# Kernel optimization log

Hardware: AMD Instinct MI355X
Metric: run time of the kernel (lower is better)

Reference implementation:

```python
import jax, jax.numpy as jnp
import numpy as np

HEAD_DEPTH = 64
CLIP = 10.0
SCALE = float(np.sqrt(HEAD_DEPTH))


def setup_inputs() -> dict:
    key = jax.random.key(0)
    kq, kk, kv, km = jax.random.split(key, 4)
    B, H, S, D = 4, 16, 2048, HEAD_DEPTH
    q = jax.random.normal(kq, (B, H, S, D), dtype=jnp.float32)
    k = jax.random.normal(kk, (B, H, S, D), dtype=jnp.float32)
    v = jax.random.normal(kv, (B, H, S, D), dtype=jnp.float32)
    # mask: (batch, n_nodes, 1) bool; True => key position is masked out
    mask = jax.random.randint(km, (B, S, 1), 0, 2).astype(bool)
    return {"q": q, "k": k, "v": v, "mask": mask}


def reference(q, k, v, mask):
    # logits: (B, H, Sq, Sk)
    logits = jnp.einsum('bhqd,bhkd->bhqk', q, k) / SCALE
    logits = CLIP * jnp.tanh(logits)  # tanh-clip of logits
    # mask (B, N, 1) -> broadcast over heads and query positions: (B, 1, 1, N)
    key_mask = mask[:, None, None, :, 0]
    logits = jnp.where(key_mask, -jnp.inf, logits)
    probs = jax.nn.softmax(logits, axis=-1)
    return jnp.einsum('bhqk,bhkd->bhqd', probs, v)
```

## Files before the change

kernel.cpp:

```cpp
#include <hip/hip_runtime.h>

typedef short bf16x8 __attribute__((ext_vector_type(8), may_alias));
typedef float f32x4 __attribute__((ext_vector_type(4)));
typedef unsigned int u32x4a __attribute__((ext_vector_type(4), may_alias));
typedef unsigned int u32x2a __attribute__((ext_vector_type(2), may_alias));
typedef unsigned short ushort;
typedef unsigned int uint;

#define B_N 4
#define H_N 16
#define S_N 2048
#define D_N 64
#define BQ 128
#define WQ 32
#define KT 64
#define NW 4
#define NBLK (B_N*H_N*(S_N/BQ))
#define TILE_BYTES 32768
#define MAXTILE (S_N/KT)
#define IMG_OFF 32768
#define WS_NEED ((size_t)IMG_OFF + (size_t)B_N*H_N*MAXTILE*TILE_BYTES)

#define MFMA16 __builtin_amdgcn_mfma_f32_16x16x32_bf16

__device__ __forceinline__ uint f2bf(float x){
  uint u = __float_as_uint(x);
  u += 0x7fffu + ((u >> 16) & 1u);
  return u >> 16;
}
__device__ __forceinline__ float bf2f(uint h){
  return __uint_as_float(h << 16);
}
__device__ __forceinline__ int ldsw(int off, int row){
  return off ^ ((row & 7) << 4);
}
__device__ __forceinline__ void gload16(const void* g, void* l){
  __builtin_amdgcn_global_load_lds((const uint __attribute__((address_space(1)))*)g,
                                   (uint __attribute__((address_space(3)))*)l, 16, 0, 0);
}

__global__ __launch_bounds__(256)
void compact_k(const int* __restrict__ Mg, int* __restrict__ cnt_ws,
               ushort* __restrict__ idx_ws)
{
  __shared__ int sws[NW];
  const int b = blockIdx.x;
  const int tid = threadIdx.x, lane = tid & 63, w = tid >> 6;
  const int* mb = Mg + (size_t)b * S_N;
  int kept[8]; int cl = 0; int base = tid * 8;
  #pragma unroll
  for (int i = 0; i < 8; ++i){ kept[i] = (mb[base+i] == 0); cl += kept[i]; }
  int inc = cl;
  #pragma unroll
  for (int d = 1; d < 64; d <<= 1){
    int o = __shfl_up(inc, d);
    if (lane >= d) inc += o;
  }
  if (lane == 63) sws[w] = inc;
  __syncthreads();
  int s0 = sws[0], s1 = sws[1], s2 = sws[2], s3 = sws[3];
  int wo = (w > 0 ? s0 : 0) + (w > 1 ? s1 : 0) + (w > 2 ? s2 : 0);
  int pos = wo + inc - cl;
  #pragma unroll
  for (int i = 0; i < 8; ++i){
    if (kept[i]) idx_ws[b*S_N + pos++] = (ushort)(base + i);
  }
  if (tid == 0) cnt_ws[b] = s0 + s1 + s2 + s3;
}

__global__ __launch_bounds__(256)
void stage_k(const float* __restrict__ Kg, const float* __restrict__ Vg,
             const int* __restrict__ cnt_ws, const ushort* __restrict__ idx_ws,
             char* __restrict__ img)
{
  __shared__ float Vl[64*65];
  const int bid = blockIdx.x;
  const int bh = bid >> 5;
  const int tile = bid & 31;
  const int b = bh >> 4;
  const int cnt = cnt_ws[b];
  const int ntile = (cnt + 63) >> 6;
  if (tile >= ntile) return;
  const int tid = threadIdx.x;
  char* G = img + (size_t)bid * TILE_BYTES;

  const int jrow = tid >> 2, c4 = tid & 3;
  int kk = tile*64 + jrow; if (kk >= cnt) kk = cnt - 1;
  const int sidx = idx_ws[b*S_N + kk];
  const size_t kvbase = (size_t)bh * (size_t)(S_N*D_N);
  const int sw = (jrow & 7) << 4;
  {
    const float4* Kp = (const float4*)(Kg + kvbase + (size_t)sidx*D_N) + c4*4;
    float4 k0 = Kp[0], k1 = Kp[1], k2 = Kp[2], k3 = Kp[3];
    float kv[16] = {k0.x,k0.y,k0.z,k0.w,k1.x,k1.y,k1.z,k1.w,
                    k2.x,k2.y,k2.z,k2.w,k3.x,k3.y,k3.z,k3.w};
    uint h[16], l[16];
    #pragma unroll
    for (int e = 0; e < 16; ++e){
      uint hh = f2bf(kv[e]); h[e] = hh; l[e] = f2bf(kv[e] - bf2f(hh));
    }
    char* r0 = G + jrow*128;
    char* r1 = G + 8192 + jrow*128;
    *(u32x4a*)(r0 + ((c4*32)      ^ sw)) = (u32x4a){h[0]|(h[1]<<16),  h[2]|(h[3]<<16),
                                                    h[4]|(h[5]<<16),  h[6]|(h[7]<<16)};
    *(u32x4a*)(r0 + ((c4*32 + 16) ^ sw)) = (u32x4a){h[8]|(h[9]<<16),  h[10]|(h[11]<<16),
                                                    h[12]|(h[13]<<16),h[14]|(h[15]<<16)};
    *(u32x4a*)(r1 + ((c4*32)      ^ sw)) = (u32x4a){l[0]|(l[1]<<16),  l[2]|(l[3]<<16),
                                                    l[4]|(l[5]<<16),  l[6]|(l[7]<<16)};
    *(u32x4a*)(r1 + ((c4*32 + 16) ^ sw)) = (u32x4a){l[8]|(l[9]<<16),  l[10]|(l[11]<<16),
                                                    l[12]|(l[13]<<16),l[14]|(l[15]<<16)};
  }
  {
    const float4* Vp = (const float4*)(Vg + kvbase + (size_t)sidx*D_N) + c4*4;
    float4 v0 = Vp[0], v1 = Vp[1], v2 = Vp[2], v3 = Vp[3];
    float vv[16] = {v0.x,v0.y,v0.z,v0.w,v1.x,v1.y,v1.z,v1.w,
                    v2.x,v2.y,v2.z,v2.w,v3.x,v3.y,v3.z,v3.w};
    #pragma unroll
    for (int e = 0; e < 16; ++e) Vl[jrow*65 + c4*16 + e] = vv[e];
  }
  __syncthreads();
  #pragma unroll
  for (int t = 0; t < 2; ++t){
    int idx2 = tid + t*256;
    int d = idx2 >> 3, g = idx2 & 7;
    int jb = (g ^ (d & 7)) * 8;
    uint hh[8], ll[8];
    #pragma unroll
    for (int e = 0; e < 8; ++e){
      float x = Vl[(jb+e)*65 + d];
      uint h = f2bf(x); hh[e] = h; ll[e] = f2bf(x - bf2f(h));
    }
    *(u32x4a*)(G + 16384 + d*128 + g*16) =
        (u32x4a){hh[0]|(hh[1]<<16), hh[2]|(hh[3]<<16), hh[4]|(hh[5]<<16), hh[6]|(hh[7]<<16)};
    *(u32x4a*)(G + 24576 + d*128 + g*16) =
        (u32x4a){ll[0]|(ll[1]<<16), ll[2]|(ll[3]<<16), ll[4]|(ll[5]<<16), ll[6]|(ll[7]<<16)};
  }
}

__global__ __launch_bounds__(256, 2)
void attn2_k(const float* __restrict__ Qg, const char* __restrict__ img,
             const int* __restrict__ cnt_ws, float* __restrict__ Og)
{
  __shared__ __align__(16) ushort smem[2][16384];
  __shared__ __align__(16) ushort Pb[NW][2][1024];

  const int tid  = threadIdx.x;
  const int lane = tid & 63;
  const int w    = tid >> 6;
  const int c    = lane & 15;
  const int gi   = lane >> 4;

  int bid = blockIdx.x;
  int wg  = (bid & 7) * (NBLK/8) + (bid >> 3);
  int qt  = wg & 15;
  int bh  = wg >> 4;
  int b   = bh >> 4;

  const int cnt = cnt_ws[b];
  const int ntile = (cnt + 63) >> 6;
  const char* Gb = img + (size_t)bh * MAXTILE * TILE_BYTES;

  if (ntile > 0){
    const char* src = Gb + w*8192 + lane*16;
    char* dst = (char*)(&smem[0][0]) + w*8192;
    #pragma unroll
    for (int i = 0; i < 8; ++i) gload16(src + i*1024, dst + i*1024);
  }

  const int q0w = qt * BQ + w * WQ;
  bf16x8 qh[2][2], ql[2][2];
  {
    const float* Qbase = Qg + (size_t)bh * S_N * D_N;
    #pragma unroll
    for (int qs = 0; qs < 2; ++qs){
      const float* qr = Qbase + (size_t)(q0w + qs*16 + c) * D_N;
      #pragma unroll
      for (int ks = 0; ks < 2; ++ks){
        const float4* p4 = (const float4*)(qr + ks*32 + gi*8);
        float4 x0 = p4[0], x1 = p4[1];
        float xs[8] = {x0.x,x0.y,x0.z,x0.w,x1.x,x1.y,x1.z,x1.w};
        union { bf16x8 v; ushort u[8]; } uh, ul;
        #pragma unroll
        for (int e = 0; e < 8; ++e){
          uint h = f2bf(xs[e]);
          uh.u[e] = (ushort)h;
          ul.u[e] = (ushort)f2bf(xs[e] - bf2f(h));
        }
        qh[qs][ks] = uh.v; ql[qs][ks] = ul.v;
      }
    }
  }

  f32x4 Oa[2][4];
  #pragma unroll
  for (int i = 0; i < 2; ++i)
    #pragma unroll
    for (int jj = 0; jj < 4; ++jj)
      Oa[i][jj] = (f32x4){0.f,0.f,0.f,0.f};
  float zz[2] = {0.f, 0.f};

  ushort* Ph = Pb[w][0];
  ushort* Pl = Pb[w][1];
  const int swc = (c & 7) << 4;
  const int e0 = (16*gi) ^ swc;
  const int e1 = (64 + 16*gi) ^ swc;

  __syncthreads();

  for (int tb = 0; tb < ntile; ++tb){
    const int buf = tb & 1;
    if (tb + 1 < ntile){
      const char* src = Gb + (size_t)(tb+1) * TILE_BYTES + w*8192 + lane*16;
      char* dst = (char*)(&smem[buf^1][0]) + w*8192;
      #pragma unroll
      for (int i = 0; i < 8; ++i) gload16(src + i*1024, dst + i*1024);
    }
    const char* Khi  = (const char*)(&smem[buf][0]);
    const char* Klo  = Khi + 8192;
    const char* VThi = Khi + 16384;
    const char* VTlo = Khi + 24576;
    const bool lastt = (tb == ntile - 1);

    #pragma unroll
    for (int qs = 0; qs < 2; ++qs){
      #pragma unroll
      for (int kt = 0; kt < 4; ++kt){
        int row = kt*16 + c;
        const char* krh = Khi + row*128;
        const char* krl = Klo + row*128;
        bf16x8 kh0 = *(const bf16x8*)(krh + e0);
        bf16x8 kh1 = *(const bf16x8*)(krh + e1);
        bf16x8 kl0 = *(const bf16x8*)(krl + e0);
        bf16x8 kl1 = *(const bf16x8*)(krl + e1);
        f32x4 s = (f32x4){0.f,0.f,0.f,0.f};
        s = MFMA16(kh0, qh[qs][0], s, 0,0,0);
        s = MFMA16(kh1, qh[qs][1], s, 0,0,0);
        s = MFMA16(kh0, ql[qs][0], s, 0,0,0);
        s = MFMA16(kh1, ql[qs][1], s, 0,0,0);
        s = MFMA16(kl0, qh[qs][0], s, 0,0,0);
        s = MFMA16(kl1, qh[qs][1], s, 0,0,0);
        float pv[4];
        #pragma unroll
        for (int r = 0; r < 4; ++r){
          float t  = __builtin_amdgcn_exp2f(s[r] * 0.3606737602222409f);
          float wv = __builtin_amdgcn_rcpf(t + 1.0f);
          pv[r] = __builtin_amdgcn_exp2f(-28.853900817779268f * wv);
        }
        if (lastt){
          int kg0 = tb*KT + kt*16 + gi*4;
          #pragma unroll
          for (int r = 0; r < 4; ++r) if (kg0 + r >= cnt) pv[r] = 0.f;
        }
        zz[qs] += (pv[0] + pv[1]) + (pv[2] + pv[3]);
        uint hA, hB, lA, lB;
        asm("v_cvt_pk_bf16_f32 %0, %1, %2" : "=v"(hA) : "v"(pv[0]), "v"(pv[1]));
        asm("v_cvt_pk_bf16_f32 %0, %1, %2" : "=v"(hB) : "v"(pv[2]), "v"(pv[3]));
        float l0 = pv[0] - __uint_as_float(hA << 16);
        float l1 = pv[1] - __uint_as_float(hA & 0xffff0000u);
        float l2 = pv[2] - __uint_as_float(hB << 16);
        float l3 = pv[3] - __uint_as_float(hB & 0xffff0000u);
        asm("v_cvt_pk_bf16_f32 %0, %1, %2" : "=v"(lA) : "v"(l0), "v"(l1));
        asm("v_cvt_pk_bf16_f32 %0, %1, %2" : "=v"(lB) : "v"(l2), "v"(l3));
        int ow = c*128 + ((kt*32 + gi*8) ^ swc);
        *(u32x2a*)((char*)Ph + ow) = (u32x2a){hA, hB};
        *(u32x2a*)((char*)Pl + ow) = (u32x2a){lA, lB};
      }
      bf16x8 pah[2], pal[2];
      {
        const char* prh = (const char*)Ph + c*128;
        const char* prl = (const char*)Pl + c*128;
        #pragma unroll
        for (int ks = 0; ks < 2; ++ks){
          int oo = (64*ks + 16*gi) ^ swc;
          pah[ks] = *(const bf16x8*)(prh + oo);
          pal[ks] = *(const bf16x8*)(prl + oo);
        }
      }
      #pragma unroll
      for (int ds = 0; ds < 4; ++ds){
        int drow = ds*16 + c;
        const char* vrh = VThi + drow*128;
        const char* vrl = VTlo + drow*128;
        f32x4 o = Oa[qs][ds];
        #pragma unroll
        for (int ks = 0; ks < 2; ++ks){
          int oo = (64*ks + 16*gi) ^ swc;
          bf16x8 vh = *(const bf16x8*)(vrh + oo);
          bf16x8 vl = *(const bf16x8*)(vrl + oo);
          o = MFMA16(pah[ks], vh, o, 0,0,0);
          o = MFMA16(pah[ks], vl, o, 0,0,0);
          o = MFMA16(pal[ks], vh, o, 0,0,0);
        }
        Oa[qs][ds] = o;
      }
    }
    __syncthreads();
  }

  #pragma unroll
  for (int qs = 0; qs < 2; ++qs){
    float zt = zz[qs];
    zt += __shfl_xor(zt, 16);
    zt += __shfl_xor(zt, 32);
    float rz = 1.0f / zt;
    #pragma unroll
    for (int r = 0; r < 4; ++r){
      float rzq = __shfl(rz, gi*4 + r);
      size_t rowbase = ((size_t)bh * S_N + (size_t)(q0w + qs*16 + gi*4 + r)) * D_N;
      #pragma unroll
      for (int ds = 0; ds < 4; ++ds){
        Og[rowbase + ds*16 + c] = Oa[qs][ds][r] * rzq;
      }
    }
  }
}

__global__ __launch_bounds__(256, 2)
void attn_k(const float* __restrict__ Qg, const float* __restrict__ Kg,
            const float* __restrict__ Vg, const int* __restrict__ Mg,
            float* __restrict__ Og)
{
  __shared__ __align__(16) ushort Khi[KT*D_N];
  __shared__ __align__(16) ushort Klo[KT*D_N];
  __shared__ __align__(16) ushort Vhi[D_N*72];
  __shared__ __align__(16) ushort Vlo[D_N*72];
  __shared__ __align__(16) ushort Phl[NW*16*72];
  __shared__ __align__(16) ushort Pll[NW*16*72];
  __shared__ ushort idx_l[S_N];
  __shared__ int scan_ws[NW];

  const int tid  = threadIdx.x;
  const int lane = tid & 63;
  const int w    = tid >> 6;
  const int c    = lane & 15;
  const int gi   = lane >> 4;

  int bid = blockIdx.x;
  int wg  = (bid & 7) * (NBLK/8) + (bid >> 3);
  int qt  = wg & 15;
  int bh  = wg >> 4;
  int b   = bh >> 4;

  int cnt;
  {
    const int* mb = Mg + (size_t)b * S_N;
    int kept[8]; int cl = 0;
    int base = tid * 8;
    #pragma unroll
    for (int i = 0; i < 8; ++i){ kept[i] = (mb[base+i] == 0); cl += kept[i]; }
    int inc = cl;
    #pragma unroll
    for (int d = 1; d < 64; d <<= 1){
      int o = __shfl_up(inc, d);
      if (lane >= d) inc += o;
    }
    if (lane == 63) scan_ws[w] = inc;
    __syncthreads();
    int s0 = scan_ws[0], s1 = scan_ws[1], s2 = scan_ws[2], s3 = scan_ws[3];
    int wo = (w > 0 ? s0 : 0) + (w > 1 ? s1 : 0) + (w > 2 ? s2 : 0);
    cnt = s0 + s1 + s2 + s3;
    int pos = wo + inc - cl;
    #pragma unroll
    for (int i = 0; i < 8; ++i){
      if (kept[i]) idx_l[pos++] = (ushort)(base + i);
    }
    __syncthreads();
  }

  const int q0w = qt * BQ + w * WQ;
  bf16x8 qh[2][2], ql[2][2];
  {
    const float* Qbase = Qg + (size_t)bh * S_N * D_N;
    #pragma unroll
    for (int qs = 0; qs < 2; ++qs){
      const float* qr = Qbase + (size_t)(q0w + qs*16 + c) * D_N;
      #pragma unroll
      for (int ks = 0; ks < 2; ++ks){
        const float4* p4 = (const float4*)(qr + ks*32 + gi*8);
        float4 x0 = p4[0], x1 = p4[1];
        float xs[8] = {x0.x,x0.y,x0.z,x0.w,x1.x,x1.y,x1.z,x1.w};
        union { bf16x8 v; ushort u[8]; } uh, ul;
        #pragma unroll
        for (int e = 0; e < 8; ++e){
          uint h = f2bf(xs[e]);
          uh.u[e] = (ushort)h;
          ul.u[e] = (ushort)f2bf(xs[e] - bf2f(h));
        }
        qh[qs][ks] = uh.v; ql[qs][ks] = ul.v;
      }
    }
  }

  f32x4 Oa[2][4];
  #pragma unroll
  for (int i = 0; i < 2; ++i)
    #pragma unroll
    for (int jj = 0; jj < 4; ++jj)
      Oa[i][jj] = (f32x4){0.f,0.f,0.f,0.f};
  float zz[2] = {0.f, 0.f};

  ushort* Ph = Phl + w * (16*72);
  ushort* Pl = Pll + w * (16*72);

  const int jrow = tid >> 2;
  const int c4   = tid & 3;
  const size_t kvbase = (size_t)bh * S_N * D_N;

  const int ntile = (cnt + KT - 1) >> 6;
  for (int tb = 0; tb < ntile; ++tb){
    {
      int kk = tb*KT + jrow;
      int ci = kk < cnt ? kk : cnt - 1;
      int sidx = idx_l[ci];
      const float4* Kp = (const float4*)(Kg + kvbase + (size_t)sidx * D_N) + c4*4;
      const float4* Vp = (const float4*)(Vg + kvbase + (size_t)sidx * D_N) + c4*4;
      float4 k0 = Kp[0], k1 = Kp[1], k2 = Kp[2], k3 = Kp[3];
      float kv[16] = {k0.x,k0.y,k0.z,k0.w,k1.x,k1.y,k1.z,k1.w,
                      k2.x,k2.y,k2.z,k2.w,k3.x,k3.y,k3.z,k3.w};
      uint kh[16], klv[16];
      #pragma unroll
      for (int e = 0; e < 16; ++e){
        uint h = f2bf(kv[e]);
        kh[e] = h; klv[e] = f2bf(kv[e] - bf2f(h));
      }
      u32x4a H0 = (u32x4a){kh[0]|(kh[1]<<16),   kh[2]|(kh[3]<<16),
                           kh[4]|(kh[5]<<16),   kh[6]|(kh[7]<<16)};
      u32x4a H1 = (u32x4a){kh[8]|(kh[9]<<16),   kh[10]|(kh[11]<<16),
                           kh[12]|(kh[13]<<16), kh[14]|(kh[15]<<16)};
      u32x4a L0 = (u32x4a){klv[0]|(klv[1]<<16),   klv[2]|(klv[3]<<16),
                           klv[4]|(klv[5]<<16),   klv[6]|(klv[7]<<16)};
      u32x4a L1 = (u32x4a){klv[8]|(klv[9]<<16),   klv[10]|(klv[11]<<16),
                           klv[12]|(klv[13]<<16), klv[14]|(klv[15]<<16)};
      char* krh = (char*)Khi + jrow*128;
      char* krl = (char*)Klo + jrow*128;
      int o0 = ldsw(c4*32, jrow), o1 = ldsw(c4*32 + 16, jrow);
      *(u32x4a*)(krh + o0) = H0;  *(u32x4a*)(krh + o1) = H1;
      *(u32x4a*)(krl + o0) = L0;  *(u32x4a*)(krl + o1) = L1;

      float4 v0 = Vp[0], v1 = Vp[1], v2 = Vp[2], v3 = Vp[3];
      float vv[16] = {v0.x,v0.y,v0.z,v0.w,v1.x,v1.y,v1.z,v1.w,
                      v2.x,v2.y,v2.z,v2.w,v3.x,v3.y,v3.z,v3.w};
      #pragma unroll
      for (int e = 0; e < 16; ++e){
        int d = c4*16 + e;
        uint h  = f2bf(vv[e]);
        uint l2 = f2bf(vv[e] - bf2f(h));
        int off = d*144 + ldsw(jrow*2, d);
        *(ushort*)((char*)Vhi + off) = (ushort)h;
        *(ushort*)((char*)Vlo + off) = (ushort)l2;
      }
    }
    __syncthreads();

    const bool lastt = (tb == ntile - 1);
    #pragma unroll
    for (int qs = 0; qs < 2; ++qs){
      #pragma unroll
      for (int kt = 0; kt < 4; ++kt){
        int row = kt*16 + c;
        const char* krh = (const char*)Khi + row*128;
        const char* krl = (const char*)Klo + row*128;
        int e0 = ldsw(16*gi, row), e1 = ldsw(64 + 16*gi, row);
        bf16x8 kh0 = *(const bf16x8*)(krh + e0);
        bf16x8 kh1 = *(const bf16x8*)(krh + e1);
        bf16x8 kl0 = *(const bf16x8*)(krl + e0);
        bf16x8 kl1 = *(const bf16x8*)(krl + e1);
        f32x4 s = (f32x4){0.f,0.f,0.f,0.f};
        s = MFMA16(kh0, qh[qs][0], s, 0,0,0);
        s = MFMA16(kh1, qh[qs][1], s, 0,0,0);
        s = MFMA16(kh0, ql[qs][0], s, 0,0,0);
        s = MFMA16(kh1, ql[qs][1], s, 0,0,0);
        s = MFMA16(kl0, qh[qs][0], s, 0,0,0);
        s = MFMA16(kl1, qh[qs][1], s, 0,0,0);
        float pv[4];
        #pragma unroll
        for (int r = 0; r < 4; ++r){
          float t  = __builtin_amdgcn_exp2f(s[r] * 0.3606737602222409f);
          float wv = __builtin_amdgcn_rcpf(t + 1.0f);
          pv[r] = __builtin_amdgcn_exp2f(-28.853900817779268f * wv);
        }
        if (lastt){
          int kg0 = tb*KT + kt*16 + gi*4;
          #pragma unroll
          for (int r = 0; r < 4; ++r) if (kg0 + r >= cnt) pv[r] = 0.f;
        }
        zz[qs] += (pv[0] + pv[1]) + (pv[2] + pv[3]);
        uint h0 = f2bf(pv[0]), h1 = f2bf(pv[1]),
             h2 = f2bf(pv[2]), h3 = f2bf(pv[3]);
        uint l0 = f2bf(pv[0]-bf2f(h0)), l1 = f2bf(pv[1]-bf2f(h1)),
             l2 = f2bf(pv[2]-bf2f(h2)), l3 = f2bf(pv[3]-bf2f(h3));
        int ow = c*144 + ldsw(kt*32 + gi*8, c);
        *(u32x2a*)((char*)Ph + ow) = (u32x2a){h0|(h1<<16), h2|(h3<<16)};
        *(u32x2a*)((char*)Pl + ow) = (u32x2a){l0|(l1<<16), l2|(l3<<16)};
      }
      bf16x8 pah[2], pal[2];
      {
        const char* prh = (const char*)Ph + c*144;
        const char* prl = (const char*)Pl + c*144;
        #pragma unroll
        for (int ks = 0; ks < 2; ++ks){
          int oo = ldsw(64*ks + 16*gi, c);
          pah[ks] = *(const bf16x8*)(prh + oo);
          pal[ks] = *(const bf16x8*)(prl + oo);
        }
      }
      #pragma unroll
      for (int ds = 0; ds < 4; ++ds){
        int drow = ds*16 + c;
        const char* vrh = (const char*)Vhi + drow*144;
        const char* vrl = (const char*)Vlo + drow*144;
        f32x4 o = Oa[qs][ds];
        #pragma unroll
        for (int ks = 0; ks < 2; ++ks){
          int oo = ldsw(64*ks + 16*gi, drow);
          bf16x8 vh = *(const bf16x8*)(vrh + oo);
          bf16x8 vl = *(const bf16x8*)(vrl + oo);
          o = MFMA16(pah[ks], vh, o, 0,0,0);
          o = MFMA16(pah[ks], vl, o, 0,0,0);
          o = MFMA16(pal[ks], vh, o, 0,0,0);
        }
        Oa[qs][ds] = o;
      }
    }
    __syncthreads();
  }

  #pragma unroll
  for (int qs = 0; qs < 2; ++qs){
    float zt = zz[qs];
    zt += __shfl_xor(zt, 16);
    zt += __shfl_xor(zt, 32);
    float rz = 1.0f / zt;
    #pragma unroll
    for (int r = 0; r < 4; ++r){
      float rzq = __shfl(rz, gi*4 + r);
      size_t rowbase = ((size_t)bh * S_N + (size_t)(q0w + qs*16 + gi*4 + r)) * D_N;
      #pragma unroll
      for (int ds = 0; ds < 4; ++ds){
        Og[rowbase + ds*16 + c] = Oa[qs][ds][r] * rzq;
      }
    }
  }
}

extern "C" void kernel_launch(void* const* d_in, const int* in_sizes, int n_in,
                              void* d_out, int out_size, void* d_ws, size_t ws_size,
                              hipStream_t stream) {
  const float* Qg = (const float*)d_in[0];
  const float* Kg = (const float*)d_in[1];
  const float* Vg = (const float*)d_in[2];
  const int*   Mg = (const int*)d_in[3];
  float* Og = (float*)d_out;
  if (ws_size >= WS_NEED){
    int*    cnt_ws = (int*)d_ws;
    ushort* idx_ws = (ushort*)((char*)d_ws + 64);
    char*   img    = (char*)d_ws + IMG_OFF;
    compact_k<<<dim3(B_N), dim3(256), 0, stream>>>(Mg, cnt_ws, idx_ws);
    stage_k<<<dim3(B_N*H_N*MAXTILE), dim3(256), 0, stream>>>(Kg, Vg, cnt_ws, idx_ws, img);
    attn2_k<<<dim3(NBLK), dim3(256), 0, stream>>>(Qg, img, cnt_ws, Og);
  } else {
    attn_k<<<dim3(NBLK), dim3(256), 0, stream>>>(Qg, Kg, Vg, Mg, Og);
  }
}
```

Measured before the change: 152.2 us.

## Halve attention key tile to 32 keys for smaller LDS and higher occupancy

The attention kernel now processes 32-key half-tiles instead of 64-key tiles. Shared memory per block is halved (double-buffered K/V half-tiles plus smaller P buffers), and launch bounds are raised from 2 to 4 blocks per SIMD to allow more concurrent workgroups. Staging uses a re-swizzled load of the transposed V half from the existing image layout. This doubles the number of loop iterations and barriers and cuts the MFMA work between syncs, in exchange for more latency hiding; the tighter register budget may cause spills.

```diff
diff --git a/kernel.cpp b/kernel.cpp
--- a/kernel.cpp
+++ b/kernel.cpp
@@ -137,12 +137,12 @@
   }
 }
 
-__global__ __launch_bounds__(256, 2)
-void attn2_k(const float* __restrict__ Qg, const char* __restrict__ img,
+__global__ __launch_bounds__(256, 4)
+void attn3_k(const float* __restrict__ Qg, const char* __restrict__ img,
              const int* __restrict__ cnt_ws, float* __restrict__ Og)
 {
-  __shared__ __align__(16) ushort smem[2][16384];
-  __shared__ __align__(16) ushort Pb[NW][2][1024];
+  __shared__ __align__(16) char smem[2][16384];
+  __shared__ __align__(16) ushort Pb[NW][2][512];
 
   const int tid  = threadIdx.x;
   const int lane = tid & 63;
@@ -157,15 +157,33 @@
   int b   = bh >> 4;
 
   const int cnt = cnt_ws[b];
-  const int ntile = (cnt + 63) >> 6;
+  const int nhalf = (cnt + 31) >> 5;
   const char* Gb = img + (size_t)bh * MAXTILE * TILE_BYTES;
 
-  if (ntile > 0){
-    const char* src = Gb + w*8192 + lane*16;
-    char* dst = (char*)(&smem[0][0]) + w*8192;
-    #pragma unroll
-    for (int i = 0; i < 8; ++i) gload16(src + i*1024, dst + i*1024);
-  }
+  auto stage = [&](int hidx, int sb){
+    const char* T = Gb + (size_t)(hidx >> 1) * TILE_BYTES;
+    const int h = hidx & 1;
+    char* Bse = (char*)&smem[sb][0];
+    if (w < 2){
+      const char* src = T + w*8192 + h*4096 + lane*16;
+      char* dst = Bse + w*4096;
+      #pragma unroll
+      for (int i = 0; i < 4; ++i) gload16(src + i*1024, dst + i*1024);
+    } else {
+      const int hl = w - 2;
+      const char* base = T + 16384 + hl*8192;
+      char* dst = Bse + 8192 + hl*4096;
+      #pragma unroll
+      for (int i = 0; i < 4; ++i){
+        int pos = i*1024 + lane*16;
+        int d = pos >> 6, p = (pos >> 4) & 3;
+        int G = (h*4 + (p ^ (d & 3))) ^ (d & 7);
+        gload16(base + d*128 + G*16, dst + pos);
+      }
+    }
+  };
+
+  if (nhalf > 0) stage(0, 0);
 
   const int q0w = qt * BQ + w * WQ;
   bf16x8 qh[2][2], ql[2][2];
@@ -199,32 +217,30 @@
       Oa[i][jj] = (f32x4){0.f,0.f,0.f,0.f};
   float zz[2] = {0.f, 0.f};
 
-  ushort* Ph = Pb[w][0];
-  ushort* Pl = Pb[w][1];
-  const int swc = (c & 7) << 4;
-  const int e0 = (16*gi) ^ swc;
-  const int e1 = (64 + 16*gi) ^ swc;
+  char* PhB = (char*)&Pb[w][0][0];
+  char* PlB = (char*)&Pb[w][1][0];
+  const int swc16 = (c & 7) << 4;
+  const int swc8  = (c & 7) << 3;
+  const int e0 = (gi*16) ^ swc16;
+  const int e1 = (64 + gi*16) ^ swc16;
+  const int po0 = (gi*16) ^ swc8;
+  const int po1 = (gi*16 + 8) ^ swc8;
 
   __syncthreads();
 
-  for (int tb = 0; tb < ntile; ++tb){
+  for (int tb = 0; tb < nhalf; ++tb){
     const int buf = tb & 1;
-    if (tb + 1 < ntile){
-      const char* src = Gb + (size_t)(tb+1) * TILE_BYTES + w*8192 + lane*16;
-      char* dst = (char*)(&smem[buf^1][0]) + w*8192;
-      #pragma unroll
-      for (int i = 0; i < 8; ++i) gload16(src + i*1024, dst + i*1024);
-    }
-    const char* Khi  = (const char*)(&smem[buf][0]);
-    const char* Klo  = Khi + 8192;
-    const char* VThi = Khi + 16384;
-    const char* VTlo = Khi + 24576;
-    const bool lastt = (tb == ntile - 1);
+    if (tb + 1 < nhalf) stage(tb + 1, buf ^ 1);
+    const char* Khi  = &smem[buf][0];
+    const char* Klo  = Khi + 4096;
+    const char* VThi = Khi + 8192;
+    const char* VTlo = Khi + 12288;
+    const bool lastt = (tb == nhalf - 1);
 
     #pragma unroll
     for (int qs = 0; qs < 2; ++qs){
       #pragma unroll
-      for (int kt = 0; kt < 4; ++kt){
+      for (int kt = 0; kt < 2; ++kt){
         int row = kt*16 + c;
         const char* krh = Khi + row*128;
         const char* krl = Klo + row*128;
@@ -247,7 +263,7 @@
           pv[r] = __builtin_amdgcn_exp2f(-28.853900817779268f * wv);
         }
         if (lastt){
-          int kg0 = tb*KT + kt*16 + gi*4;
+          int kg0 = tb*32 + kt*16 + gi*4;
           #pragma unroll
           for (int r = 0; r < 4; ++r) if (kg0 + r >= cnt) pv[r] = 0.f;
         }
@@ -261,36 +277,26 @@
         float l3 = pv[3] - __uint_as_float(hB & 0xffff0000u);
         asm("v_cvt_pk_bf16_f32 %0, %1, %2" : "=v"(lA) : "v"(l0), "v"(l1));
         asm("v_cvt_pk_bf16_f32 %0, %1, %2" : "=v"(lB) : "v"(l2), "v"(l3));
-        int ow = c*128 + ((kt*32 + gi*8) ^ swc);
-        *(u32x2a*)((char*)Ph + ow) = (u32x2a){hA, hB};
-        *(u32x2a*)((char*)Pl + ow) = (u32x2a){lA, lB};
-      }
-      bf16x8 pah[2], pal[2];
-      {
-        const char* prh = (const char*)Ph + c*128;
-        const char* prl = (const char*)Pl + c*128;
-        #pragma unroll
-        for (int ks = 0; ks < 2; ++ks){
-          int oo = (64*ks + 16*gi) ^ swc;
-          pah[ks] = *(const bf16x8*)(prh + oo);
-          pal[ks] = *(const bf16x8*)(prl + oo);
-        }
-      }
+        int ow = c*64 + ((kt*32 + gi*8) ^ swc8);
+        *(u32x2a*)(PhB + ow) = (u32x2a){hA, hB};
+        *(u32x2a*)(PlB + ow) = (u32x2a){lA, lB};
+      }
+      union PU { bf16x8 v; u32x2a g[2]; };
+      PU pah, pal;
+      pah.g[0] = *(const u32x2a*)(PhB + c*64 + po0);
+      pah.g[1] = *(const u32x2a*)(PhB + c*64 + po1);
+      pal.g[0] = *(const u32x2a*)(PlB + c*64 + po0);
+      pal.g[1] = *(const u32x2a*)(PlB + c*64 + po1);
       #pragma unroll
       for (int ds = 0; ds < 4; ++ds){
         int drow = ds*16 + c;
-        const char* vrh = VThi + drow*128;
-        const char* vrl = VTlo + drow*128;
+        int va = (gi*16) ^ ((drow & 3) << 4);
+        bf16x8 vh = *(const bf16x8*)(VThi + drow*64 + va);
+        bf16x8 vl = *(const bf16x8*)(VTlo + drow*64 + va);
         f32x4 o = Oa[qs][ds];
-        #pragma unroll
-        for (int ks = 0; ks < 2; ++ks){
-          int oo = (64*ks + 16*gi) ^ swc;
-          bf16x8 vh = *(const bf16x8*)(vrh + oo);
-          bf16x8 vl = *(const bf16x8*)(vrl + oo);
-          o = MFMA16(pah[ks], vh, o, 0,0,0);
-          o = MFMA16(pah[ks], vl, o, 0,0,0);
-          o = MFMA16(pal[ks], vh, o, 0,0,0);
-        }
+        o = MFMA16(pah.v, vh, o, 0,0,0);
+        o = MFMA16(pah.v, vl, o, 0,0,0);
+        o = MFMA16(pal.v, vh, o, 0,0,0);
         Oa[qs][ds] = o;
       }
     }
@@ -557,7 +563,7 @@
     char*   img    = (char*)d_ws + IMG_OFF;
     compact_k<<<dim3(B_N), dim3(256), 0, stream>>>(Mg, cnt_ws, idx_ws);
     stage_k<<<dim3(B_N*H_N*MAXTILE), dim3(256), 0, stream>>>(Kg, Vg, cnt_ws, idx_ws, img);
-    attn2_k<<<dim3(NBLK), dim3(256), 0, stream>>>(Qg, img, cnt_ws, Og);
+    attn3_k<<<dim3(NBLK), dim3(256), 0, stream>>>(Qg, img, cnt_ws, Og);
   } else {
     attn_k<<<dim3(NBLK), dim3(256), 0, stream>>>(Qg, Kg, Vg, Mg, Og);
   }
```

Result: slower. 213.8 us (+40.5%).
